# Optimization experiments

Hardware: AMD Instinct MI355X
Metric: run time of the kernel (lower is better)

The kernel has to match this reference:

```python
import jax, jax.numpy as jnp
import numpy as np
from jax import lax
import math

LAYERS, STACKS = 10, 3
NL = LAYERS * STACKS          # 30 residual layers
DC, RC, SC, CLASSES, K = 32, 32, 256, 256, 2


def _conv1d(x, w, b, dilation=1, pad_left=0):
    # x: [B, Cin, T], w: [Cout, Cin, Kw]. Left-padding by (Kw-1)*dilation
    # reproduces torch's symmetric pad followed by x[:, :, :T] (causal conv).
    out = lax.conv_general_dilated(
        x, w, window_strides=(1,), padding=[(pad_left, 0)],
        rhs_dilation=(dilation,), dimension_numbers=('NCH', 'OIH', 'NCH'))
    return out + b[None, :, None]


def setup_inputs() -> dict:
    key = jax.random.key(0)
    ks = jax.random.split(key, 13)
    B, T = 4, 32768
    s = jnp.float32(0.05)
    return {
        'y': jax.random.normal(ks[0], (B, CLASSES, T), jnp.float32),
        'W_causal': jax.random.normal(ks[1], (RC, CLASSES, 1)) * s,
        'b_causal': jax.random.normal(ks[2], (RC,)) * s,
        'Wf': jax.random.normal(ks[3], (NL, DC, RC, K)) * s,
        'bf': jax.random.normal(ks[4], (NL, DC)) * s,
        'Wr': jax.random.normal(ks[5], (NL, RC, DC // 2, 1)) * s,
        'br': jax.random.normal(ks[6], (NL, RC)) * s,
        'Ws': jax.random.normal(ks[7], (NL, SC, DC // 2, 1)) * s,
        'bs': jax.random.normal(ks[8], (NL, SC)) * s,
        'W_e1': jax.random.normal(ks[9], (SC, SC, 1)) * s,
        'b_e1': jax.random.normal(ks[10], (SC,)) * s,
        'W_e2': jax.random.normal(ks[11], (CLASSES, SC, 1)) * s,
        'b_e2': jax.random.normal(ks[12], (CLASSES,)) * s,
    }


def reference(y, W_causal, b_causal, Wf, bf, Wr, br, Ws, bs, W_e1, b_e1, W_e2, b_e2):
    # y: [B, 256, T]
    x = _conv1d(y, W_causal, b_causal)                      # [B, RC, T]
    skip = jnp.zeros((y.shape[0], SC, y.shape[2]), y.dtype)
    inv_sqrt2 = jnp.float32(math.sqrt(0.5))
    for i in range(NL):  # fixed 30 structurally distinct layers (dilation varies)
        d = 2 ** (i % LAYERS)
        residual = x
        h = _conv1d(x, Wf[i], bf[i], dilation=d, pad_left=(K - 1) * d)  # [B, DC, T]
        a, b = jnp.split(h, 2, axis=1)                      # each [B, DC//2, T]
        g = jnp.tanh(a) * jax.nn.sigmoid(b)
        skip = skip + _conv1d(g, Ws[i], bs[i])              # [B, SC, T]
        x = (_conv1d(g, Wr[i], br[i]) + residual) * inv_sqrt2
    x = jax.nn.relu(skip)
    x = jax.nn.relu(_conv1d(x, W_e1, b_e1))
    x = _conv1d(x, W_e2, b_e2)                              # [B, CLASSES, T]
    return jnp.transpose(x, (0, 2, 1))                      # [B, T, CLASSES]
```

## Files before the change

kernel.cpp:

```cpp
#include <hip/hip_runtime.h>
#include <hip/hip_bf16.h>


#define B_ 4
#define T_ 32768
#define RC_ 32
#define KH_ 16
#define SC_ 256
#define CLASSES_ 256
#define NL_ 30
#define NT_ 131072L

using f32x4 = __attribute__((ext_vector_type(4))) float;
using s16x8 = __attribute__((ext_vector_type(8))) short;

__device__ inline float fast_rcp(float x) { return __builtin_amdgcn_rcpf(x); }
__device__ inline float fast_sigmoid(float x) { return fast_rcp(1.f + __expf(-x)); }
__device__ inline float fast_tanh(float x) { return 1.f - 2.f * fast_rcp(__expf(2.f * x) + 1.f); }

__device__ inline ushort f2bf(float v) {
    __hip_bfloat16 h = __float2bfloat16(v);
    return __builtin_bit_cast(ushort, h);
}
__device__ inline uint pack2(float a, float b) {
    return (uint)f2bf(a) | ((uint)f2bf(b) << 16);
}
__device__ inline float bflo(uint u) { return __builtin_bit_cast(float, u << 16); }
__device__ inline float bfhi(uint u) { return __builtin_bit_cast(float, u & 0xffff0000u); }
__device__ inline s16x8 mfma_in(uint4 u) { return __builtin_bit_cast(s16x8, u); }

__global__ __launch_bounds__(256) void prep_w_kernel(
    const float* __restrict__ Wc, const float* __restrict__ Wf,
    const float* __restrict__ Wr, const float* __restrict__ Ws,
    const float* __restrict__ We1, const float* __restrict__ We2,
    ushort* __restrict__ wcp, ushort* __restrict__ wfp, ushort* __restrict__ wrp,
    ushort* __restrict__ wsF, ushort* __restrict__ we1F, ushort* __restrict__ we2F)
{
    int j = blockIdx.x * 256 + threadIdx.x;
    if (j < 24576) {
        int m = j / 768, k = j % 768;
        float v = Wc[m * 256 + (k & 255)];
        if (k < 512) wcp[j] = f2bf(v);
        else {
            float hi = __bfloat162float(__float2bfloat16(v));
            wcp[j] = f2bf(v - hi);
        }
    } else if (j < 86016) {
        int e = j - 24576;
        int i = e >> 11; int r = e & 2047;
        int tap = r >> 10, c = (r >> 5) & 31, ci = r & 31;
        wfp[e] = f2bf(Wf[((size_t)(i * 32 + c) * 32 + ci) * 2 + tap]);
    } else if (j < 116736) {
        int e = j - 86016;
        int i = e >> 10; int c = (e >> 5) & 31; int k = e & 31;
        wrp[e] = (k < 16) ? f2bf(Wr[(size_t)(i * 32 + c) * 16 + k]) : (ushort)0;
    } else if (j < 239616) {
        int e = j - 116736;
        int jj = e & 7, lane = (e >> 3) & 63, mrow = (e >> 9) & 15, kc = e >> 13;
        int m = mrow * 16 + (lane & 15);
        int k = kc * 32 + (lane >> 4) * 8 + jj;
        int i = k >> 4, ci = k & 15;
        wsF[e] = f2bf(Ws[((size_t)i * 256 + m) * 16 + ci]);
    } else if (j < 305152) {
        int e = j - 239616;
        int jj = e & 7, lane = (e >> 3) & 63, mrow = (e >> 9) & 15, kc = e >> 13;
        int m = mrow * 16 + (lane & 15);
        int k = kc * 32 + (lane >> 4) * 8 + jj;
        we1F[e] = f2bf(We1[m * 256 + k]);
    } else if (j < 370688) {
        int e = j - 305152;
        int jj = e & 7, lane = (e >> 3) & 63, mrow = (e >> 9) & 15, kc = e >> 13;
        int m = mrow * 16 + (lane & 15);
        int k = kc * 32 + (lane >> 4) * 8 + jj;
        we2F[e] = f2bf(We2[m * 256 + k]);
    }
}

__global__ void bsum_kernel(const float* __restrict__ bs, float* __restrict__ bsSum) {
    int s = threadIdx.x;
    float v = 0.f;
    #pragma unroll
    for (int i = 0; i < NL_; ++i) v += bs[i * SC_ + s];
    bsSum[s] = v;
}

__global__ __launch_bounds__(256) void prep_y_kernel(
    const float* __restrict__ y, ushort* __restrict__ y_t)
{
    __shared__ float lds[32][65];
    int tid = threadIdx.x;
    int b = blockIdx.x >> 9;
    long t0 = (long)(blockIdx.x & 511) * 64;
    for (int cc = 0; cc < 8; ++cc) {
        int c = cc * 32 + (tid >> 3);
        int tp = (tid & 7) * 8;
        const float* src = y + ((size_t)b * 256 + c) * T_ + t0 + tp;
        float4 v0 = *(const float4*)src;
        float4 v1 = *(const float4*)(src + 4);
        lds[tid >> 3][tp + 0] = v0.x; lds[tid >> 3][tp + 1] = v0.y;
        lds[tid >> 3][tp + 2] = v0.z; lds[tid >> 3][tp + 3] = v0.w;
        lds[tid >> 3][tp + 4] = v1.x; lds[tid >> 3][tp + 5] = v1.y;
        lds[tid >> 3][tp + 6] = v1.z; lds[tid >> 3][tp + 7] = v1.w;
        __syncthreads();
        int t = tid & 63, cp = tid >> 6;
        float v[8];
        #pragma unroll
        for (int jj = 0; jj < 8; ++jj) v[jj] = lds[cp * 8 + jj][t];
        uint hi[4], lo[4];
        #pragma unroll
        for (int jj = 0; jj < 4; ++jj) {
            float a = v[2 * jj], bv = v[2 * jj + 1];
            float ah = __bfloat162float(__float2bfloat16(a));
            float bh = __bfloat162float(__float2bfloat16(bv));
            hi[jj] = pack2(a, bv);
            lo[jj] = pack2(a - ah, bv - bh);
        }
        ushort* dst = y_t + ((size_t)b * T_ + t0 + t) * 512 + cc * 32 + cp * 8;
        *(uint4*)dst = make_uint4(hi[0], hi[1], hi[2], hi[3]);
        *(uint4*)(dst + 256) = make_uint4(lo[0], lo[1], lo[2], lo[3]);
        __syncthreads();
    }
}

__global__ __launch_bounds__(256) void init_gemm_kernel(
    const ushort* __restrict__ wcp, const ushort* __restrict__ y_t,
    const float* __restrict__ bc, ushort* __restrict__ x0)
{
    __shared__ ushort sa[2][32 * 40];
    __shared__ ushort sb[2][256 * 40];
    int tid = threadIdx.x;
    int wid = tid >> 6, lane = tid & 63, q = lane >> 4, ln = lane & 15;
    long n0 = (long)blockIdx.x * 256;

    uint4 ar0, ar1, br0, br1, br2, br3;
    auto load_tile = [&](int kc) {
        int k0 = kc * 32;
        int koff = (k0 < 512) ? k0 : k0 - 512;
        if (tid < 64) {
            int m = tid >> 1, h = tid & 1;
            const uint4* s = (const uint4*)(wcp + m * 768 + k0 + h * 16);
            ar0 = s[0]; ar1 = s[1];
        }
        const uint4* sB = (const uint4*)(y_t + (n0 + tid) * 512 + koff);
        br0 = sB[0]; br1 = sB[1]; br2 = sB[2]; br3 = sB[3];
    };
    auto store_tile = [&](int buf) {
        if (tid < 64) {
            int m = tid >> 1, h = tid & 1;
            *(uint4*)&sa[buf][m * 40 + h * 16] = ar0;
            *(uint4*)&sa[buf][m * 40 + h * 16 + 8] = ar1;
        }
        *(uint4*)&sb[buf][tid * 40 + 0]  = br0;
        *(uint4*)&sb[buf][tid * 40 + 8]  = br1;
        *(uint4*)&sb[buf][tid * 40 + 16] = br2;
        *(uint4*)&sb[buf][tid * 40 + 24] = br3;
    };

    f32x4 acc[2][4];
    #pragma unroll
    for (int mi = 0; mi < 2; ++mi) {
        f32x4 bv = *(const f32x4*)&bc[mi * 16 + 4 * q];
        #pragma unroll
        for (int ni = 0; ni < 4; ++ni) acc[mi][ni] = bv;
    }
    load_tile(0);
    for (int kc = 0; kc < 24; ++kc) {
        int buf = kc & 1;
        store_tile(buf);
        __syncthreads();
        if (kc + 1 < 24) load_tile(kc + 1);
        s16x8 af[2];
        #pragma unroll
        for (int mi = 0; mi < 2; ++mi)
            af[mi] = mfma_in(*(const uint4*)&sa[buf][(mi * 16 + ln) * 40 + q * 8]);
        #pragma unroll
        for (int ni = 0; ni < 4; ++ni) {
            s16x8 bfr = mfma_in(*(const uint4*)&sb[buf][(wid * 64 + ni * 16 + ln) * 40 + q * 8]);
            #pragma unroll
            for (int mi = 0; mi < 2; ++mi)
                acc[mi][ni] = __builtin_amdgcn_mfma_f32_16x16x32_bf16(af[mi], bfr, acc[mi][ni], 0, 0, 0);
        }
        __syncthreads();
    }
    #pragma unroll
    for (int mi = 0; mi < 2; ++mi) {
        int ch = mi * 16 + 4 * q;
        #pragma unroll
        for (int ni = 0; ni < 4; ++ni) {
            long t = n0 + wid * 64 + ni * 16 + ln;
            f32x4 v = acc[mi][ni];
            uint2 pk; pk.x = pack2(v[0], v[1]); pk.y = pack2(v[2], v[3]);
            *(uint2*)&x0[t * 32 + ch] = pk;
        }
    }
}

__global__ __launch_bounds__(256) void layer_mfma_kernel(
    const ushort* __restrict__ xb_in, ushort* __restrict__ xb_out,
    ushort* __restrict__ g_out,
    const ushort* __restrict__ wfp, const ushort* __restrict__ wrp,
    const float* __restrict__ bfp, const float* __restrict__ brp, int d)
{
    int tid = threadIdx.x;
    int wid = tid >> 6, lane = tid & 63, q = lane >> 4, ln = lane & 15;
    long tw = (long)blockIdx.x * 128 + wid * 32;

    s16x8 wfA[2][2], wrA[2];
    #pragma unroll
    for (int mb = 0; mb < 2; ++mb) {
        #pragma unroll
        for (int tap = 0; tap < 2; ++tap)
            wfA[mb][tap] = mfma_in(*(const uint4*)&wfp[(tap * 32 + mb * 16 + ln) * 32 + q * 8]);
        wrA[mb] = mfma_in(*(const uint4*)&wrp[(mb * 16 + ln) * 32 + q * 8]);
    }
    f32x4 bfv0 = *(const f32x4*)&bfp[4 * q];
    f32x4 bfv1 = *(const f32x4*)&bfp[16 + 4 * q];
    f32x4 brv0 = *(const f32x4*)&brp[4 * q];
    f32x4 brv1 = *(const f32x4*)&brp[16 + 4 * q];
    const float inv_s2 = 0.70710678118654752f;

    #pragma unroll
    for (int nb = 0; nb < 2; ++nb) {
        long t = tw + nb * 16 + ln;
        bool vok = ((int)(t & (T_ - 1)) >= d);
        long r0 = vok ? (t - d) : t;
        uint4 u0 = *(const uint4*)&xb_in[r0 * 32 + 8 * q];
        if (!vok) u0 = make_uint4(0, 0, 0, 0);
        uint4 u1 = *(const uint4*)&xb_in[t * 32 + 8 * q];
        s16x8 b0 = mfma_in(u0), b1 = mfma_in(u1);

        f32x4 h0 = {}, h1 = {};
        h0 = __builtin_amdgcn_mfma_f32_16x16x32_bf16(wfA[0][0], b0, h0, 0, 0, 0);
        h0 = __builtin_amdgcn_mfma_f32_16x16x32_bf16(wfA[0][1], b1, h0, 0, 0, 0);
        h1 = __builtin_amdgcn_mfma_f32_16x16x32_bf16(wfA[1][0], b0, h1, 0, 0, 0);
        h1 = __builtin_amdgcn_mfma_f32_16x16x32_bf16(wfA[1][1], b1, h1, 0, 0, 0);

        float g[4];
        #pragma unroll
        for (int r = 0; r < 4; ++r)
            g[r] = fast_tanh(h0[r] + bfv0[r]) * fast_sigmoid(h1[r] + bfv1[r]);
        uint p01 = pack2(g[0], g[1]), p23 = pack2(g[2], g[3]);
        uint2 gst; gst.x = p01; gst.y = p23;
        *(uint2*)&g_out[t * 16 + 4 * q] = gst;

        int sA = q * 32 + ln;
        uint f0 = (uint)__shfl((int)p01, sA);
        uint f1 = (uint)__shfl((int)p23, sA);
        uint f2 = (uint)__shfl((int)p01, sA + 16);
        uint f3 = (uint)__shfl((int)p23, sA + 16);
        s16x8 gb = mfma_in(make_uint4(f0, f1, f2, f3));

        f32x4 rr0 = {}, rr1 = {};
        rr0 = __builtin_amdgcn_mfma_f32_16x16x32_bf16(wrA[0], gb, rr0, 0, 0, 0);
        rr1 = __builtin_amdgcn_mfma_f32_16x16x32_bf16(wrA[1], gb, rr1, 0, 0, 0);

        uint2 xr0 = *(const uint2*)&xb_in[t * 32 + 4 * q];
        uint2 xr1 = *(const uint2*)&xb_in[t * 32 + 16 + 4 * q];
        float o00 = (rr0[0] + brv0[0] + bflo(xr0.x)) * inv_s2;
        float o01 = (rr0[1] + brv0[1] + bfhi(xr0.x)) * inv_s2;
        float o02 = (rr0[2] + brv0[2] + bflo(xr0.y)) * inv_s2;
        float o03 = (rr0[3] + brv0[3] + bfhi(xr0.y)) * inv_s2;
        float o10 = (rr1[0] + brv1[0] + bflo(xr1.x)) * inv_s2;
        float o11 = (rr1[1] + brv1[1] + bfhi(xr1.x)) * inv_s2;
        float o12 = (rr1[2] + brv1[2] + bflo(xr1.y)) * inv_s2;
        float o13 = (rr1[3] + brv1[3] + bfhi(xr1.y)) * inv_s2;
        uint2 xp0; xp0.x = pack2(o00, o01); xp0.y = pack2(o02, o03);
        uint2 xp1; xp1.x = pack2(o10, o11); xp1.y = pack2(o12, o13);
        *(uint2*)&xb_out[t * 32 + 4 * q] = xp0;
        *(uint2*)&xb_out[t * 32 + 16 + 4 * q] = xp1;
    }
}

__global__ __launch_bounds__(256, 4) void tail_kernel(
    const ushort* __restrict__ g_all, const float* __restrict__ bsSum,
    const ushort* __restrict__ wsF, const ushort* __restrict__ we1F,
    const ushort* __restrict__ we2F, const float* __restrict__ be1,
    const float* __restrict__ be2, float* __restrict__ out)
{
    __shared__ ushort stg[2][2048];
    __shared__ ushort pq[16384];
    int tid = threadIdx.x;
    int wid = tid >> 6, lane = tid & 63, q = lane >> 4, ln = lane & 15;
    long n0 = (long)blockIdx.x * 64;
    int wrow = wid * 64;

    int sn = tid & 63, sip = (tid >> 6) & 1, shalf = tid >> 7;
    int sdst = ((sn >> 4) * 64 + (sip * 2 + shalf) * 16 + (sn & 15)) * 8;

    f32x4 acc[4][4];
    #pragma unroll
    for (int mi = 0; mi < 4; ++mi) {
        f32x4 bv = *(const f32x4*)&bsSum[wrow + mi * 16 + 4 * q];
        #pragma unroll
        for (int ni = 0; ni < 4; ++ni) acc[mi][ni] = bv;
    }

    uint4 ld = *(const uint4*)(g_all + ((size_t)sip * NT_ + n0 + sn) * 16 + shalf * 8);
    *(uint4*)&stg[0][sdst] = ld;
    for (int kc = 0; kc < 15; ++kc) {
        __syncthreads();
        if (kc < 14)
            ld = *(const uint4*)(g_all +
                ((size_t)(2 * (kc + 1) + sip) * NT_ + n0 + sn) * 16 + shalf * 8);
        s16x8 af[4], bfr[4];
        #pragma unroll
        for (int mi = 0; mi < 4; ++mi)
            af[mi] = mfma_in(*(const uint4*)(wsF +
                (((size_t)kc * 16 + wid * 4 + mi) * 64 + lane) * 8));
        #pragma unroll
        for (int ni = 0; ni < 4; ++ni)
            bfr[ni] = mfma_in(*(const uint4*)&stg[kc & 1][(ni * 64 + lane) * 8]);
        #pragma unroll
        for (int ni = 0; ni < 4; ++ni)
            #pragma unroll
            for (int mi = 0; mi < 4; ++mi)
                acc[mi][ni] = __builtin_amdgcn_mfma_f32_16x16x32_bf16(
                    af[mi], bfr[ni], acc[mi][ni], 0, 0, 0);
        if (kc < 14) *(uint4*)&stg[(kc + 1) & 1][sdst] = ld;
    }
    #pragma unroll
    for (int mi = 0; mi < 4; ++mi) {
        int ch = wrow + mi * 16 + 4 * q;
        int dbase = ((ch >> 5) * 4) * 512 + (((ch & 31) >> 3) * 16 + ln) * 8 + (ch & 7);
        #pragma unroll
        for (int ni = 0; ni < 4; ++ni) {
            f32x4 v = acc[mi][ni];
            uint2 pk;
            pk.x = pack2(fmaxf(v[0], 0.f), fmaxf(v[1], 0.f));
            pk.y = pack2(fmaxf(v[2], 0.f), fmaxf(v[3], 0.f));
            *(uint2*)&pq[dbase + ni * 512] = pk;
        }
    }
    __syncthreads();

    #pragma unroll
    for (int mi = 0; mi < 4; ++mi) {
        f32x4 bv = *(const f32x4*)&be1[wrow + mi * 16 + 4 * q];
        #pragma unroll
        for (int ni = 0; ni < 4; ++ni) acc[mi][ni] = bv;
    }
    for (int kc = 0; kc < 8; ++kc) {
        s16x8 af[4], bfr[4];
        #pragma unroll
        for (int mi = 0; mi < 4; ++mi)
            af[mi] = mfma_in(*(const uint4*)(we1F +
                (((size_t)kc * 16 + wid * 4 + mi) * 64 + lane) * 8));
        #pragma unroll
        for (int ni = 0; ni < 4; ++ni)
            bfr[ni] = mfma_in(*(const uint4*)&pq[(kc * 4 + ni) * 512 + lane * 8]);
        #pragma unroll
        for (int ni = 0; ni < 4; ++ni)
            #pragma unroll
            for (int mi = 0; mi < 4; ++mi)
                acc[mi][ni] = __builtin_amdgcn_mfma_f32_16x16x32_bf16(
                    af[mi], bfr[ni], acc[mi][ni], 0, 0, 0);
    }
    __syncthreads();
    #pragma unroll
    for (int mi = 0; mi < 4; ++mi) {
        int ch = wrow + mi * 16 + 4 * q;
        int dbase = ((ch >> 5) * 4) * 512 + (((ch & 31) >> 3) * 16 + ln) * 8 + (ch & 7);
        #pragma unroll
        for (int ni = 0; ni < 4; ++ni) {
            f32x4 v = acc[mi][ni];
            uint2 pk;
            pk.x = pack2(fmaxf(v[0], 0.f), fmaxf(v[1], 0.f));
            pk.y = pack2(fmaxf(v[2], 0.f), fmaxf(v[3], 0.f));
            *(uint2*)&pq[dbase + ni * 512] = pk;
        }
    }
    __syncthreads();

    #pragma unroll
    for (int mi = 0; mi < 4; ++mi) {
        f32x4 bv = *(const f32x4*)&be2[wrow + mi * 16 + 4 * q];
        #pragma unroll
        for (int ni = 0; ni < 4; ++ni) acc[mi][ni] = bv;
    }
    for (int kc = 0; kc < 8; ++kc) {
        s16x8 af[4], bfr[4];
        #pragma unroll
        for (int mi = 0; mi < 4; ++mi)
            af[mi] = mfma_in(*(const uint4*)(we2F +
                (((size_t)kc * 16 + wid * 4 + mi) * 64 + lane) * 8));
        #pragma unroll
        for (int ni = 0; ni < 4; ++ni)
            bfr[ni] = mfma_in(*(const uint4*)&pq[(kc * 4 + ni) * 512 + lane * 8]);
        #pragma unroll
        for (int ni = 0; ni < 4; ++ni)
            #pragma unroll
            for (int mi = 0; mi < 4; ++mi)
                acc[mi][ni] = __builtin_amdgcn_mfma_f32_16x16x32_bf16(
                    af[mi], bfr[ni], acc[mi][ni], 0, 0, 0);
    }
    #pragma unroll
    for (int mi = 0; mi < 4; ++mi) {
        int ch = wrow + mi * 16 + 4 * q;
        #pragma unroll
        for (int ni = 0; ni < 4; ++ni) {
            long t = n0 + ni * 16 + ln;
            *(f32x4*)&out[t * 256 + ch] = acc[mi][ni];
        }
    }
}

__device__ inline float load_g(const float* p) { return *p; }
__device__ inline float load_g(const __hip_bfloat16* p) { return __bfloat162float(*p); }
__device__ inline void store_g(float* p, float v) { *p = v; }
__device__ inline void store_g(__hip_bfloat16* p, float v) { *p = __float2bfloat16(v); }

__global__ __launch_bounds__(256) void init_conv_kernel(
    const float* __restrict__ y, const float* __restrict__ Wc,
    const float* __restrict__ bc, float* __restrict__ x0)
{
    int gid = blockIdx.x * 256 + threadIdx.x;
    int b = gid >> 15;
    int t = gid & (T_ - 1);
    float acc[RC_];
    #pragma unroll
    for (int c = 0; c < RC_; ++c) acc[c] = bc[c];
    const float* yb = y + (size_t)b * CLASSES_ * T_ + t;
    for (int cb = 0; cb < CLASSES_; cb += 32) {
        float yv[32];
        #pragma unroll
        for (int j = 0; j < 32; ++j) yv[j] = yb[(size_t)(cb + j) * T_];
        #pragma unroll
        for (int c = 0; c < RC_; ++c)
            #pragma unroll
            for (int j = 0; j < 32; ++j)
                acc[c] = fmaf(Wc[c * CLASSES_ + cb + j], yv[j], acc[c]);
    }
    float* xo = x0 + (size_t)b * RC_ * T_ + t;
    #pragma unroll
    for (int c = 0; c < RC_; ++c) xo[(size_t)c * T_] = acc[c];
}

template <typename G>
__global__ __launch_bounds__(256) void layer_kernel(
    const float* __restrict__ x_in, float* __restrict__ x_out, G* __restrict__ g_out,
    const float* __restrict__ wf, const float* __restrict__ bfp,
    const float* __restrict__ wr, const float* __restrict__ brp, int d)
{
    int gid = blockIdx.x * 256 + threadIdx.x;
    int b = gid >> 15;
    int t = gid & (T_ - 1);
    const float* xbase = x_in + (size_t)b * RC_ * T_ + t;
    float xm[RC_], xd[RC_];
    #pragma unroll
    for (int ci = 0; ci < RC_; ++ci) xm[ci] = xbase[(size_t)ci * T_];
    #pragma unroll
    for (int ci = 0; ci < RC_; ++ci)
        xd[ci] = (t >= d) ? xbase[(size_t)ci * T_ - d] : 0.f;
    float a_[KH_];
    #pragma unroll
    for (int c = 0; c < KH_; ++c) {
        float s = bfp[c];
        #pragma unroll
        for (int ci = 0; ci < RC_; ++ci) {
            s = fmaf(wf[(c * RC_ + ci) * 2 + 0], xd[ci], s);
            s = fmaf(wf[(c * RC_ + ci) * 2 + 1], xm[ci], s);
        }
        a_[c] = s;
    }
    float g[KH_];
    #pragma unroll
    for (int c = 0; c < KH_; ++c) {
        float s = bfp[KH_ + c];
        #pragma unroll
        for (int ci = 0; ci < RC_; ++ci) {
            s = fmaf(wf[((KH_ + c) * RC_ + ci) * 2 + 0], xd[ci], s);
            s = fmaf(wf[((KH_ + c) * RC_ + ci) * 2 + 1], xm[ci], s);
        }
        g[c] = fast_tanh(a_[c]) * fast_sigmoid(s);
    }
    G* gb = g_out + (size_t)b * KH_ * T_ + t;
    #pragma unroll
    for (int c = 0; c < KH_; ++c) store_g(gb + (size_t)c * T_, g[c]);
    float* xo = x_out + (size_t)b * RC_ * T_ + t;
    #pragma unroll
    for (int c = 0; c < RC_; ++c) {
        float s = brp[c];
        #pragma unroll
        for (int ci = 0; ci < KH_; ++ci) s = fmaf(wr[c * KH_ + ci], g[ci], s);
        xo[(size_t)c * T_] = (s + xm[c]) * 0.70710678118654752f;
    }
}

template <typename G>
__global__ __launch_bounds__(256) void final_kernel(
    const G* __restrict__ g_all, const float* __restrict__ bsSum,
    const float* __restrict__ Ws, const float* __restrict__ We1,
    const float* __restrict__ be1, const float* __restrict__ We2,
    const float* __restrict__ be2, float* __restrict__ out)
{
    __shared__ float smem[14336];
    float* plds = smem;
    float* qlds = smem + 5120;
    float* glds = smem;
    float* wlds = smem + 10240;
    int tid = threadIdx.x;
    int bt = blockIdx.x;
    int b = bt >> 11;
    int t0 = (bt & 2047) << 4;
    int c4 = tid & 63;
    int th = tid >> 6;
    for (int e = tid; e < 480 * 16; e += 256) {
        int row = e >> 4, col = e & 15;
        int i = row >> 4, ci = row & 15;
        glds[e] = load_g(g_all + ((size_t)(i * B_ + b) * KH_ + ci) * T_ + t0 + col);
    }
    __syncthreads();
    float acc[4][4];
    #pragma unroll
    for (int j = 0; j < 4; ++j) {
        float bv = bsSum[c4 + 64 * j];
        #pragma unroll
        for (int tt = 0; tt < 4; ++tt) acc[j][tt] = bv;
    }
    for (int i = 0; i < NL_; ++i) {
        const float4* wsrc = (const float4*)(Ws + ((size_t)i * 256 + tid) * 16);
        float4 w0 = wsrc[0], w1 = wsrc[1], w2 = wsrc[2], w3 = wsrc[3];
        __syncthreads();
        wlds[0*256+tid]=w0.x; wlds[1*256+tid]=w0.y; wlds[2*256+tid]=w0.z; wlds[3*256+tid]=w0.w;
        wlds[4*256+tid]=w1.x; wlds[5*256+tid]=w1.y; wlds[6*256+tid]=w1.z; wlds[7*256+tid]=w1.w;
        wlds[8*256+tid]=w2.x; wlds[9*256+tid]=w2.y; wlds[10*256+tid]=w2.z; wlds[11*256+tid]=w2.w;
        wlds[12*256+tid]=w3.x; wlds[13*256+tid]=w3.y; wlds[14*256+tid]=w3.z; wlds[15*256+tid]=w3.w;
        __syncthreads();
        #pragma unroll
        for (int ci = 0; ci < 16; ++ci) {
            const float4 gv = *(const float4*)&glds[(i * 16 + ci) * 16 + th * 4];
            float wv[4];
            #pragma unroll
            for (int j = 0; j < 4; ++j) wv[j] = wlds[ci * 256 + c4 + 64 * j];
            #pragma unroll
            for (int j = 0; j < 4; ++j) {
                acc[j][0] = fmaf(wv[j], gv.x, acc[j][0]);
                acc[j][1] = fmaf(wv[j], gv.y, acc[j][1]);
                acc[j][2] = fmaf(wv[j], gv.z, acc[j][2]);
                acc[j][3] = fmaf(wv[j], gv.w, acc[j][3]);
            }
        }
    }
    __syncthreads();
    #pragma unroll
    for (int j = 0; j < 4; ++j)
        #pragma unroll
        for (int tt = 0; tt < 4; ++tt)
            plds[(c4 + 64 * j) * 20 + th * 4 + tt] = fmaxf(acc[j][tt], 0.f);
    #pragma unroll
    for (int j = 0; j < 4; ++j) {
        float bv = be1[c4 + 64 * j];
        #pragma unroll
        for (int tt = 0; tt < 4; ++tt) acc[j][tt] = bv;
    }
    for (int kc = 0; kc < 16; ++kc) {
        const float4* wsrc = (const float4*)(We1 + (size_t)tid * 256 + kc * 16);
        float4 w0 = wsrc[0], w1 = wsrc[1], w2 = wsrc[2], w3 = wsrc[3];
        __syncthreads();
        wlds[0*256+tid]=w0.x; wlds[1*256+tid]=w0.y; wlds[2*256+tid]=w0.z; wlds[3*256+tid]=w0.w;
        wlds[4*256+tid]=w1.x; wlds[5*256+tid]=w1.y; wlds[6*256+tid]=w1.z; wlds[7*256+tid]=w1.w;
        wlds[8*256+tid]=w2.x; wlds[9*256+tid]=w2.y; wlds[10*256+tid]=w2.z; wlds[11*256+tid]=w2.w;
        wlds[12*256+tid]=w3.x; wlds[13*256+tid]=w3.y; wlds[14*256+tid]=w3.z; wlds[15*256+tid]=w3.w;
        __syncthreads();
        #pragma unroll
        for (int kk = 0; kk < 16; ++kk) {
            const float4 pv = *(const float4*)&plds[(kc * 16 + kk) * 20 + th * 4];
            float wv[4];
            #pragma unroll
            for (int j = 0; j < 4; ++j) wv[j] = wlds[kk * 256 + c4 + 64 * j];
            #pragma unroll
            for (int j = 0; j < 4; ++j) {
                acc[j][0] = fmaf(wv[j], pv.x, acc[j][0]);
                acc[j][1] = fmaf(wv[j], pv.y, acc[j][1]);
                acc[j][2] = fmaf(wv[j], pv.z, acc[j][2]);
                acc[j][3] = fmaf(wv[j], pv.w, acc[j][3]);
            }
        }
    }
    __syncthreads();
    #pragma unroll
    for (int j = 0; j < 4; ++j)
        #pragma unroll
        for (int tt = 0; tt < 4; ++tt)
            qlds[(c4 + 64 * j) * 20 + th * 4 + tt] = fmaxf(acc[j][tt], 0.f);
    #pragma unroll
    for (int j = 0; j < 4; ++j) {
        float bv = be2[c4 + 64 * j];
        #pragma unroll
        for (int tt = 0; tt < 4; ++tt) acc[j][tt] = bv;
    }
    for (int kc = 0; kc < 16; ++kc) {
        const float4* wsrc = (const float4*)(We2 + (size_t)tid * 256 + kc * 16);
        float4 w0 = wsrc[0], w1 = wsrc[1], w2 = wsrc[2], w3 = wsrc[3];
        __syncthreads();
        wlds[0*256+tid]=w0.x; wlds[1*256+tid]=w0.y; wlds[2*256+tid]=w0.z; wlds[3*256+tid]=w0.w;
        wlds[4*256+tid]=w1.x; wlds[5*256+tid]=w1.y; wlds[6*256+tid]=w1.z; wlds[7*256+tid]=w1.w;
        wlds[8*256+tid]=w2.x; wlds[9*256+tid]=w2.y; wlds[10*256+tid]=w2.z; wlds[11*256+tid]=w2.w;
        wlds[12*256+tid]=w3.x; wlds[13*256+tid]=w3.y; wlds[14*256+tid]=w3.z; wlds[15*256+tid]=w3.w;
        __syncthreads();
        #pragma unroll
        for (int kk = 0; kk < 16; ++kk) {
            const float4 qv = *(const float4*)&qlds[(kc * 16 + kk) * 20 + th * 4];
            float wv[4];
            #pragma unroll
            for (int j = 0; j < 4; ++j) wv[j] = wlds[kk * 256 + c4 + 64 * j];
            #pragma unroll
            for (int j = 0; j < 4; ++j) {
                acc[j][0] = fmaf(wv[j], qv.x, acc[j][0]);
                acc[j][1] = fmaf(wv[j], qv.y, acc[j][1]);
                acc[j][2] = fmaf(wv[j], qv.z, acc[j][2]);
                acc[j][3] = fmaf(wv[j], qv.w, acc[j][3]);
            }
        }
    }
    #pragma unroll
    for (int tt = 0; tt < 4; ++tt) {
        size_t orow = ((size_t)b * T_ + t0 + th * 4 + tt) * 256;
        #pragma unroll
        for (int j = 0; j < 4; ++j)
            out[orow + c4 + 64 * j] = acc[j][tt];
    }
}

template <typename G>
static void run_pipeline_old(const float* y, const float* Wc, const float* bc,
                             const float* Wf, const float* bf, const float* Wr,
                             const float* br, const float* Ws, const float* bs,
                             const float* We1, const float* be1, const float* We2,
                             const float* be2, float* out, char* ws, hipStream_t stream)
{
    size_t xbytes = (size_t)B_ * RC_ * T_ * sizeof(float);
    float* xa = (float*)ws;
    float* xb = (float*)(ws + xbytes);
    G* g_all = (G*)(ws + 2 * xbytes);
    size_t gbytes = (size_t)NL_ * B_ * KH_ * T_ * sizeof(G);
    float* bsSum = (float*)(ws + 2 * xbytes + gbytes);
    bsum_kernel<<<1, 256, 0, stream>>>(bs, bsSum);
    init_conv_kernel<<<512, 256, 0, stream>>>(y, Wc, bc, xa);
    float* xin = xa; float* xout = xb;
    for (int i = 0; i < NL_; ++i) {
        int d = 1 << (i % 10);
        layer_kernel<G><<<512, 256, 0, stream>>>(
            xin, xout, g_all + (size_t)i * B_ * KH_ * T_,
            Wf + (size_t)i * RC_ * RC_ * 2, bf + (size_t)i * RC_,
            Wr + (size_t)i * RC_ * KH_, br + (size_t)i * RC_, d);
        float* tmp = xin; xin = xout; xout = tmp;
    }
    final_kernel<G><<<B_ * (T_ / 16), 256, 0, stream>>>(
        g_all, bsSum, Ws, We1, be1, We2, be2, out);
}

extern "C" void kernel_launch(void* const* d_in, const int* in_sizes, int n_in,
                              void* d_out, int out_size, void* d_ws, size_t ws_size,
                              hipStream_t stream)
{
    (void)in_sizes; (void)n_in; (void)out_size;
    const float* y   = (const float*)d_in[0];
    const float* Wc  = (const float*)d_in[1];
    const float* bc  = (const float*)d_in[2];
    const float* Wf  = (const float*)d_in[3];
    const float* bf  = (const float*)d_in[4];
    const float* Wr  = (const float*)d_in[5];
    const float* br  = (const float*)d_in[6];
    const float* Ws  = (const float*)d_in[7];
    const float* bs  = (const float*)d_in[8];
    const float* We1 = (const float*)d_in[9];
    const float* be1 = (const float*)d_in[10];
    const float* We2 = (const float*)d_in[11];
    const float* be2 = (const float*)d_in[12];
    float* out = (float*)d_out;
    char* ws = (char*)d_ws;

    size_t o = 0;
    auto alloc = [&](size_t bytes) { size_t r = o; o += (bytes + 1023) & ~(size_t)1023; return r; };
    size_t o_reg = alloc(NT_ * 512 * 2);
    size_t o_xa  = alloc(NT_ * 32 * 2);
    size_t o_xb  = alloc(NT_ * 32 * 2);
    size_t o_wcp = alloc(24576 * 2);
    size_t o_wfp = alloc(61440 * 2);
    size_t o_wrp = alloc(30720 * 2);
    size_t o_wst = alloc(122880 * 2);
    size_t o_we1 = alloc(65536 * 2);
    size_t o_we2 = alloc(65536 * 2);
    size_t o_bss = alloc(1024);
    size_t need_new = o;

    if (ws_size >= need_new) {
        ushort* y_t  = (ushort*)(ws + o_reg);
        ushort* g    = (ushort*)(ws + o_reg);
        ushort* xba  = (ushort*)(ws + o_xa);
        ushort* xbb  = (ushort*)(ws + o_xb);
        ushort* wcp  = (ushort*)(ws + o_wcp);
        ushort* wfp  = (ushort*)(ws + o_wfp);
        ushort* wrp  = (ushort*)(ws + o_wrp);
        ushort* wsF  = (ushort*)(ws + o_wst);
        ushort* we1F = (ushort*)(ws + o_we1);
        ushort* we2F = (ushort*)(ws + o_we2);
        float*  bsSum= (float*)(ws + o_bss);

        prep_w_kernel<<<1448, 256, 0, stream>>>(Wc, Wf, Wr, Ws, We1, We2,
                                                wcp, wfp, wrp, wsF, we1F, we2F);
        bsum_kernel<<<1, 256, 0, stream>>>(bs, bsSum);
        prep_y_kernel<<<2048, 256, 0, stream>>>(y, y_t);
        init_gemm_kernel<<<512, 256, 0, stream>>>(wcp, y_t, bc, xba);

        ushort* xbin = xba; ushort* xbout = xbb;
        for (int i = 0; i < NL_; ++i) {
            int d = 1 << (i % 10);
            layer_mfma_kernel<<<1024, 256, 0, stream>>>(
                xbin, xbout, g + (size_t)i * NT_ * 16,
                wfp + (size_t)i * 2048, wrp + (size_t)i * 1024,
                bf + i * 32, br + i * 32, d);
            ushort* tmp = xbin; xbin = xbout; xbout = tmp;
        }

        tail_kernel<<<2048, 256, 0, stream>>>(g, bsSum, wsF, we1F, we2F,
                                              be1, be2, out);
        return;
    }

    size_t xbytes = (size_t)B_ * RC_ * T_ * sizeof(float);
    size_t need_f32 = 2 * xbytes + (size_t)NL_ * B_ * KH_ * T_ * 4 + 1024;
    if (ws_size >= need_f32)
        run_pipeline_old<float>(y, Wc, bc, Wf, bf, Wr, br, Ws, bs, We1, be1, We2, be2, out, ws, stream);
    else
        run_pipeline_old<__hip_bfloat16>(y, Wc, bc, Wf, bf, Wr, br, Ws, bs, We1, be1, We2, be2, out, ws, stream);
}
```

Before: 690.6 us.

## Fuse first seven dilated layers per stack into one LDS-resident kernel

Adds a stack kernel that loads a 256-step time tile plus a 128-step causal halo into shared memory and runs the first seven layers of each stack (dilations 1..64) there, exchanging x between double-buffered LDS tiles instead of global memory. Only the gate outputs and the final x are written out, and the last three layers still use the per-layer kernel. This removes the global x round trips and launches for those layers but recomputes the halo region and adds barriers. The tail kernel's output store now goes through shared memory so global writes are coalesced rows, and the fallback fp32 path is deleted.

```diff
diff --git a/kernel.cpp b/kernel.cpp
--- a/kernel.cpp
+++ b/kernel.cpp
@@ -195,6 +195,112 @@
     }
 }
 
+__global__ __launch_bounds__(256) void stack_kernel(
+    const ushort* __restrict__ xb_in, ushort* __restrict__ xb_out,
+    ushort* __restrict__ g_out,
+    const ushort* __restrict__ wfp,
+    const ushort* __restrict__ wrp,
+    const float* __restrict__ bfp, const float* __restrict__ brp)
+{
+    __shared__ ushort xl[2][384 * 40];
+    int tid = threadIdx.x;
+    int wid = tid >> 6, lane = tid & 63, q = lane >> 4, ln = lane & 15;
+    long bo = (long)blockIdx.x * 256;
+
+    #pragma unroll
+    for (int k = 0; k < 6; ++k) {
+        int idx = k * 256 + tid;
+        int row = idx >> 2, part = idx & 3;
+        long t = bo - 128 + row;
+        if (t < 0) t = 0;
+        uint4 v = *(const uint4*)&xb_in[t * 32 + part * 8];
+        *(uint4*)&xl[0][row * 40 + part * 8] = v;
+    }
+    __syncthreads();
+
+    const float inv_s2 = 0.70710678118654752f;
+    int cur = 0;
+    for (int j = 0; j < 7; ++j) {
+        int d = 1 << j;
+        s16x8 wfA[2][2], wrA[2];
+        #pragma unroll
+        for (int mb = 0; mb < 2; ++mb) {
+            #pragma unroll
+            for (int tap = 0; tap < 2; ++tap)
+                wfA[mb][tap] = mfma_in(*(const uint4*)&wfp[(size_t)j * 2048 +
+                    (tap * 32 + mb * 16 + ln) * 32 + q * 8]);
+            wrA[mb] = mfma_in(*(const uint4*)&wrp[(size_t)j * 1024 + (mb * 16 + ln) * 32 + q * 8]);
+        }
+        f32x4 bfv0 = *(const f32x4*)&bfp[j * 32 + 4 * q];
+        f32x4 bfv1 = *(const f32x4*)&bfp[j * 32 + 16 + 4 * q];
+        f32x4 brv0 = *(const f32x4*)&brp[j * 32 + 4 * q];
+        f32x4 brv1 = *(const f32x4*)&brp[j * 32 + 16 + 4 * q];
+        ushort* ga = g_out + (size_t)j * NT_ * 16;
+
+        #pragma unroll
+        for (int nb = 0; nb < 6; ++nb) {
+            int tb = wid * 96 + nb * 16;
+            int tl = tb + ln;
+            long t = bo - 128 + tl;
+            bool vok = ((int)(t & (T_ - 1)) >= d);
+            int rd = tl - d; if (rd < 0) rd = 0;
+            uint4 u0 = *(const uint4*)&xl[cur][rd * 40 + 8 * q];
+            if (!vok) u0 = make_uint4(0, 0, 0, 0);
+            uint4 u1 = *(const uint4*)&xl[cur][tl * 40 + 8 * q];
+            s16x8 b0 = mfma_in(u0), b1 = mfma_in(u1);
+
+            f32x4 h0 = {}, h1 = {};
+            h0 = __builtin_amdgcn_mfma_f32_16x16x32_bf16(wfA[0][0], b0, h0, 0, 0, 0);
+            h0 = __builtin_amdgcn_mfma_f32_16x16x32_bf16(wfA[0][1], b1, h0, 0, 0, 0);
+            h1 = __builtin_amdgcn_mfma_f32_16x16x32_bf16(wfA[1][0], b0, h1, 0, 0, 0);
+            h1 = __builtin_amdgcn_mfma_f32_16x16x32_bf16(wfA[1][1], b1, h1, 0, 0, 0);
+
+            float g[4];
+            #pragma unroll
+            for (int r = 0; r < 4; ++r)
+                g[r] = fast_tanh(h0[r] + bfv0[r]) * fast_sigmoid(h1[r] + bfv1[r]);
+            uint p01 = pack2(g[0], g[1]), p23 = pack2(g[2], g[3]);
+            if (tb >= 128) {
+                uint2 gst; gst.x = p01; gst.y = p23;
+                *(uint2*)&ga[t * 16 + 4 * q] = gst;
+            }
+
+            int sA = q * 32 + ln;
+            uint f0 = (uint)__shfl((int)p01, sA);
+            uint f1 = (uint)__shfl((int)p23, sA);
+            uint f2 = (uint)__shfl((int)p01, sA + 16);
+            uint f3 = (uint)__shfl((int)p23, sA + 16);
+            s16x8 gb = mfma_in(make_uint4(f0, f1, f2, f3));
+
+            f32x4 rr0 = {}, rr1 = {};
+            rr0 = __builtin_amdgcn_mfma_f32_16x16x32_bf16(wrA[0], gb, rr0, 0, 0, 0);
+            rr1 = __builtin_amdgcn_mfma_f32_16x16x32_bf16(wrA[1], gb, rr1, 0, 0, 0);
+
+            uint2 xr0 = *(const uint2*)&xl[cur][tl * 40 + 4 * q];
+            uint2 xr1 = *(const uint2*)&xl[cur][tl * 40 + 16 + 4 * q];
+            float o00 = (rr0[0] + brv0[0] + bflo(xr0.x)) * inv_s2;
+            float o01 = (rr0[1] + brv0[1] + bfhi(xr0.x)) * inv_s2;
+            float o02 = (rr0[2] + brv0[2] + bflo(xr0.y)) * inv_s2;
+            float o03 = (rr0[3] + brv0[3] + bfhi(xr0.y)) * inv_s2;
+            float o10 = (rr1[0] + brv1[0] + bflo(xr1.x)) * inv_s2;
+            float o11 = (rr1[1] + brv1[1] + bfhi(xr1.x)) * inv_s2;
+            float o12 = (rr1[2] + brv1[2] + bflo(xr1.y)) * inv_s2;
+            float o13 = (rr1[3] + brv1[3] + bfhi(xr1.y)) * inv_s2;
+            uint2 xp0; xp0.x = pack2(o00, o01); xp0.y = pack2(o02, o03);
+            uint2 xp1; xp1.x = pack2(o10, o11); xp1.y = pack2(o12, o13);
+            if (j < 6) {
+                *(uint2*)&xl[cur ^ 1][tl * 40 + 4 * q] = xp0;
+                *(uint2*)&xl[cur ^ 1][tl * 40 + 16 + 4 * q] = xp1;
+            } else if (tb >= 128) {
+                *(uint2*)&xb_out[t * 32 + 4 * q] = xp0;
+                *(uint2*)&xb_out[t * 32 + 16 + 4 * q] = xp1;
+            }
+        }
+        __syncthreads();
+        cur ^= 1;
+    }
+}
+
 __global__ __launch_bounds__(256) void layer_mfma_kernel(
     const ushort* __restrict__ xb_in, ushort* __restrict__ xb_out,
     ushort* __restrict__ g_out,
@@ -393,268 +499,30 @@
                 acc[mi][ni] = __builtin_amdgcn_mfma_f32_16x16x32_bf16(
                     af[mi], bfr[ni], acc[mi][ni], 0, 0, 0);
     }
-    #pragma unroll
-    for (int mi = 0; mi < 4; ++mi) {
-        int ch = wrow + mi * 16 + 4 * q;
-        #pragma unroll
-        for (int ni = 0; ni < 4; ++ni) {
-            long t = n0 + ni * 16 + ln;
-            *(f32x4*)&out[t * 256 + ch] = acc[mi][ni];
-        }
-    }
-}
-
-__device__ inline float load_g(const float* p) { return *p; }
-__device__ inline float load_g(const __hip_bfloat16* p) { return __bfloat162float(*p); }
-__device__ inline void store_g(float* p, float v) { *p = v; }
-__device__ inline void store_g(__hip_bfloat16* p, float v) { *p = __float2bfloat16(v); }
-
-__global__ __launch_bounds__(256) void init_conv_kernel(
-    const float* __restrict__ y, const float* __restrict__ Wc,
-    const float* __restrict__ bc, float* __restrict__ x0)
-{
-    int gid = blockIdx.x * 256 + threadIdx.x;
-    int b = gid >> 15;
-    int t = gid & (T_ - 1);
-    float acc[RC_];
-    #pragma unroll
-    for (int c = 0; c < RC_; ++c) acc[c] = bc[c];
-    const float* yb = y + (size_t)b * CLASSES_ * T_ + t;
-    for (int cb = 0; cb < CLASSES_; cb += 32) {
-        float yv[32];
-        #pragma unroll
-        for (int j = 0; j < 32; ++j) yv[j] = yb[(size_t)(cb + j) * T_];
-        #pragma unroll
-        for (int c = 0; c < RC_; ++c)
-            #pragma unroll
-            for (int j = 0; j < 32; ++j)
-                acc[c] = fmaf(Wc[c * CLASSES_ + cb + j], yv[j], acc[c]);
-    }
-    float* xo = x0 + (size_t)b * RC_ * T_ + t;
-    #pragma unroll
-    for (int c = 0; c < RC_; ++c) xo[(size_t)c * T_] = acc[c];
-}
-
-template <typename G>
-__global__ __launch_bounds__(256) void layer_kernel(
-    const float* __restrict__ x_in, float* __restrict__ x_out, G* __restrict__ g_out,
-    const float* __restrict__ wf, const float* __restrict__ bfp,
-    const float* __restrict__ wr, const float* __restrict__ brp, int d)
-{
-    int gid = blockIdx.x * 256 + threadIdx.x;
-    int b = gid >> 15;
-    int t = gid & (T_ - 1);
-    const float* xbase = x_in + (size_t)b * RC_ * T_ + t;
-    float xm[RC_], xd[RC_];
-    #pragma unroll
-    for (int ci = 0; ci < RC_; ++ci) xm[ci] = xbase[(size_t)ci * T_];
-    #pragma unroll
-    for (int ci = 0; ci < RC_; ++ci)
-        xd[ci] = (t >= d) ? xbase[(size_t)ci * T_ - d] : 0.f;
-    float a_[KH_];
-    #pragma unroll
-    for (int c = 0; c < KH_; ++c) {
-        float s = bfp[c];
-        #pragma unroll
-        for (int ci = 0; ci < RC_; ++ci) {
-            s = fmaf(wf[(c * RC_ + ci) * 2 + 0], xd[ci], s);
-            s = fmaf(wf[(c * RC_ + ci) * 2 + 1], xm[ci], s);
-        }
-        a_[c] = s;
-    }
-    float g[KH_];
-    #pragma unroll
-    for (int c = 0; c < KH_; ++c) {
-        float s = bfp[KH_ + c];
-        #pragma unroll
-        for (int ci = 0; ci < RC_; ++ci) {
-            s = fmaf(wf[((KH_ + c) * RC_ + ci) * 2 + 0], xd[ci], s);
-            s = fmaf(wf[((KH_ + c) * RC_ + ci) * 2 + 1], xm[ci], s);
-        }
-        g[c] = fast_tanh(a_[c]) * fast_sigmoid(s);
-    }
-    G* gb = g_out + (size_t)b * KH_ * T_ + t;
-    #pragma unroll
-    for (int c = 0; c < KH_; ++c) store_g(gb + (size_t)c * T_, g[c]);
-    float* xo = x_out + (size_t)b * RC_ * T_ + t;
-    #pragma unroll
-    for (int c = 0; c < RC_; ++c) {
-        float s = brp[c];
-        #pragma unroll
-        for (int ci = 0; ci < KH_; ++ci) s = fmaf(wr[c * KH_ + ci], g[ci], s);
-        xo[(size_t)c * T_] = (s + xm[c]) * 0.70710678118654752f;
-    }
-}
-
-template <typename G>
-__global__ __launch_bounds__(256) void final_kernel(
-    const G* __restrict__ g_all, const float* __restrict__ bsSum,
-    const float* __restrict__ Ws, const float* __restrict__ We1,
-    const float* __restrict__ be1, const float* __restrict__ We2,
-    const float* __restrict__ be2, float* __restrict__ out)
-{
-    __shared__ float smem[14336];
-    float* plds = smem;
-    float* qlds = smem + 5120;
-    float* glds = smem;
-    float* wlds = smem + 10240;
-    int tid = threadIdx.x;
-    int bt = blockIdx.x;
-    int b = bt >> 11;
-    int t0 = (bt & 2047) << 4;
-    int c4 = tid & 63;
-    int th = tid >> 6;
-    for (int e = tid; e < 480 * 16; e += 256) {
-        int row = e >> 4, col = e & 15;
-        int i = row >> 4, ci = row & 15;
-        glds[e] = load_g(g_all + ((size_t)(i * B_ + b) * KH_ + ci) * T_ + t0 + col);
-    }
-    __syncthreads();
-    float acc[4][4];
-    #pragma unroll
-    for (int j = 0; j < 4; ++j) {
-        float bv = bsSum[c4 + 64 * j];
-        #pragma unroll
-        for (int tt = 0; tt < 4; ++tt) acc[j][tt] = bv;
-    }
-    for (int i = 0; i < NL_; ++i) {
-        const float4* wsrc = (const float4*)(Ws + ((size_t)i * 256 + tid) * 16);
-        float4 w0 = wsrc[0], w1 = wsrc[1], w2 = wsrc[2], w3 = wsrc[3];
-        __syncthreads();
-        wlds[0*256+tid]=w0.x; wlds[1*256+tid]=w0.y; wlds[2*256+tid]=w0.z; wlds[3*256+tid]=w0.w;
-        wlds[4*256+tid]=w1.x; wlds[5*256+tid]=w1.y; wlds[6*256+tid]=w1.z; wlds[7*256+tid]=w1.w;
-        wlds[8*256+tid]=w2.x; wlds[9*256+tid]=w2.y; wlds[10*256+tid]=w2.z; wlds[11*256+tid]=w2.w;
-        wlds[12*256+tid]=w3.x; wlds[13*256+tid]=w3.y; wlds[14*256+tid]=w3.z; wlds[15*256+tid]=w3.w;
-        __syncthreads();
-        #pragma unroll
-        for (int ci = 0; ci < 16; ++ci) {
-            const float4 gv = *(const float4*)&glds[(i * 16 + ci) * 16 + th * 4];
-            float wv[4];
-            #pragma unroll
-            for (int j = 0; j < 4; ++j) wv[j] = wlds[ci * 256 + c4 + 64 * j];
-            #pragma unroll
-            for (int j = 0; j < 4; ++j) {
-                acc[j][0] = fmaf(wv[j], gv.x, acc[j][0]);
-                acc[j][1] = fmaf(wv[j], gv.y, acc[j][1]);
-                acc[j][2] = fmaf(wv[j], gv.z, acc[j][2]);
-                acc[j][3] = fmaf(wv[j], gv.w, acc[j][3]);
-            }
-        }
-    }
-    __syncthreads();
-    #pragma unroll
-    for (int j = 0; j < 4; ++j)
-        #pragma unroll
-        for (int tt = 0; tt < 4; ++tt)
-            plds[(c4 + 64 * j) * 20 + th * 4 + tt] = fmaxf(acc[j][tt], 0.f);
-    #pragma unroll
-    for (int j = 0; j < 4; ++j) {
-        float bv = be1[c4 + 64 * j];
-        #pragma unroll
-        for (int tt = 0; tt < 4; ++tt) acc[j][tt] = bv;
-    }
-    for (int kc = 0; kc < 16; ++kc) {
-        const float4* wsrc = (const float4*)(We1 + (size_t)tid * 256 + kc * 16);
-        float4 w0 = wsrc[0], w1 = wsrc[1], w2 = wsrc[2], w3 = wsrc[3];
-        __syncthreads();
-        wlds[0*256+tid]=w0.x; wlds[1*256+tid]=w0.y; wlds[2*256+tid]=w0.z; wlds[3*256+tid]=w0.w;
-        wlds[4*256+tid]=w1.x; wlds[5*256+tid]=w1.y; wlds[6*256+tid]=w1.z; wlds[7*256+tid]=w1.w;
-        wlds[8*256+tid]=w2.x; wlds[9*256+tid]=w2.y; wlds[10*256+tid]=w2.z; wlds[11*256+tid]=w2.w;
-        wlds[12*256+tid]=w3.x; wlds[13*256+tid]=w3.y; wlds[14*256+tid]=w3.z; wlds[15*256+tid]=w3.w;
-        __syncthreads();
-        #pragma unroll
-        for (int kk = 0; kk < 16; ++kk) {
-            const float4 pv = *(const float4*)&plds[(kc * 16 + kk) * 20 + th * 4];
-            float wv[4];
-            #pragma unroll
-            for (int j = 0; j < 4; ++j) wv[j] = wlds[kk * 256 + c4 + 64 * j];
-            #pragma unroll
-            for (int j = 0; j < 4; ++j) {
-                acc[j][0] = fmaf(wv[j], pv.x, acc[j][0]);
-                acc[j][1] = fmaf(wv[j], pv.y, acc[j][1]);
-                acc[j][2] = fmaf(wv[j], pv.z, acc[j][2]);
-                acc[j][3] = fmaf(wv[j], pv.w, acc[j][3]);
-            }
-        }
-    }
-    __syncthreads();
-    #pragma unroll
-    for (int j = 0; j < 4; ++j)
-        #pragma unroll
-        for (int tt = 0; tt < 4; ++tt)
-            qlds[(c4 + 64 * j) * 20 + th * 4 + tt] = fmaxf(acc[j][tt], 0.f);
-    #pragma unroll
-    for (int j = 0; j < 4; ++j) {
-        float bv = be2[c4 + 64 * j];
-        #pragma unroll
-        for (int tt = 0; tt < 4; ++tt) acc[j][tt] = bv;
-    }
-    for (int kc = 0; kc < 16; ++kc) {
-        const float4* wsrc = (const float4*)(We2 + (size_t)tid * 256 + kc * 16);
-        float4 w0 = wsrc[0], w1 = wsrc[1], w2 = wsrc[2], w3 = wsrc[3];
-        __syncthreads();
-        wlds[0*256+tid]=w0.x; wlds[1*256+tid]=w0.y; wlds[2*256+tid]=w0.z; wlds[3*256+tid]=w0.w;
-        wlds[4*256+tid]=w1.x; wlds[5*256+tid]=w1.y; wlds[6*256+tid]=w1.z; wlds[7*256+tid]=w1.w;
-        wlds[8*256+tid]=w2.x; wlds[9*256+tid]=w2.y; wlds[10*256+tid]=w2.z; wlds[11*256+tid]=w2.w;
-        wlds[12*256+tid]=w3.x; wlds[13*256+tid]=w3.y; wlds[14*256+tid]=w3.z; wlds[15*256+tid]=w3.w;
-        __syncthreads();
-        #pragma unroll
-        for (int kk = 0; kk < 16; ++kk) {
-            const float4 qv = *(const float4*)&qlds[(kc * 16 + kk) * 20 + th * 4];
-            float wv[4];
-            #pragma unroll
-            for (int j = 0; j < 4; ++j) wv[j] = wlds[kk * 256 + c4 + 64 * j];
-            #pragma unroll
-            for (int j = 0; j < 4; ++j) {
-                acc[j][0] = fmaf(wv[j], qv.x, acc[j][0]);
-                acc[j][1] = fmaf(wv[j], qv.y, acc[j][1]);
-                acc[j][2] = fmaf(wv[j], qv.z, acc[j][2]);
-                acc[j][3] = fmaf(wv[j], qv.w, acc[j][3]);
-            }
-        }
-    }
-    #pragma unroll
-    for (int tt = 0; tt < 4; ++tt) {
-        size_t orow = ((size_t)b * T_ + t0 + th * 4 + tt) * 256;
-        #pragma unroll
-        for (int j = 0; j < 4; ++j)
-            out[orow + c4 + 64 * j] = acc[j][tt];
-    }
-}
-
-template <typename G>
-static void run_pipeline_old(const float* y, const float* Wc, const float* bc,
-                             const float* Wf, const float* bf, const float* Wr,
-                             const float* br, const float* Ws, const float* bs,
-                             const float* We1, const float* be1, const float* We2,
-                             const float* be2, float* out, char* ws, hipStream_t stream)
-{
-    size_t xbytes = (size_t)B_ * RC_ * T_ * sizeof(float);
-    float* xa = (float*)ws;
-    float* xb = (float*)(ws + xbytes);
-    G* g_all = (G*)(ws + 2 * xbytes);
-    size_t gbytes = (size_t)NL_ * B_ * KH_ * T_ * sizeof(G);
-    float* bsSum = (float*)(ws + 2 * xbytes + gbytes);
-    bsum_kernel<<<1, 256, 0, stream>>>(bs, bsSum);
-    init_conv_kernel<<<512, 256, 0, stream>>>(y, Wc, bc, xa);
-    float* xin = xa; float* xout = xb;
-    for (int i = 0; i < NL_; ++i) {
-        int d = 1 << (i % 10);
-        layer_kernel<G><<<512, 256, 0, stream>>>(
-            xin, xout, g_all + (size_t)i * B_ * KH_ * T_,
-            Wf + (size_t)i * RC_ * RC_ * 2, bf + (size_t)i * RC_,
-            Wr + (size_t)i * RC_ * KH_, br + (size_t)i * RC_, d);
-        float* tmp = xin; xin = xout; xout = tmp;
-    }
-    final_kernel<G><<<B_ * (T_ / 16), 256, 0, stream>>>(
-        g_all, bsSum, Ws, We1, be1, We2, be2, out);
+
+    float* pqf = (float*)pq;
+    #pragma unroll
+    for (int c = 0; c < 4; ++c) {
+        __syncthreads();
+        #pragma unroll
+        for (int mi = 0; mi < 4; ++mi)
+            *(f32x4*)&pqf[ln * 260 + wrow + mi * 16 + 4 * q] = acc[mi][c];
+        __syncthreads();
+        #pragma unroll
+        for (int k = 0; k < 4; ++k) {
+            int pos = k * 256 + tid;
+            int row = pos >> 6, col = (pos & 63) * 4;
+            *(f32x4*)&out[(n0 + c * 16 + row) * 256 + col] =
+                *(const f32x4*)&pqf[row * 260 + col];
+        }
+    }
 }
 
 extern "C" void kernel_launch(void* const* d_in, const int* in_sizes, int n_in,
                               void* d_out, int out_size, void* d_ws, size_t ws_size,
                               hipStream_t stream)
 {
-    (void)in_sizes; (void)n_in; (void)out_size;
+    (void)in_sizes; (void)n_in; (void)out_size; (void)ws_size;
     const float* y   = (const float*)d_in[0];
     const float* Wc  = (const float*)d_in[1];
     const float* bc  = (const float*)d_in[2];
@@ -683,46 +551,44 @@
     size_t o_we1 = alloc(65536 * 2);
     size_t o_we2 = alloc(65536 * 2);
     size_t o_bss = alloc(1024);
-    size_t need_new = o;
-
-    if (ws_size >= need_new) {
-        ushort* y_t  = (ushort*)(ws + o_reg);
-        ushort* g    = (ushort*)(ws + o_reg);
-        ushort* xba  = (ushort*)(ws + o_xa);
-        ushort* xbb  = (ushort*)(ws + o_xb);
-        ushort* wcp  = (ushort*)(ws + o_wcp);
-        ushort* wfp  = (ushort*)(ws + o_wfp);
-        ushort* wrp  = (ushort*)(ws + o_wrp);
-        ushort* wsF  = (ushort*)(ws + o_wst);
-        ushort* we1F = (ushort*)(ws + o_we1);
-        ushort* we2F = (ushort*)(ws + o_we2);
-        float*  bsSum= (float*)(ws + o_bss);
-
-        prep_w_kernel<<<1448, 256, 0, stream>>>(Wc, Wf, Wr, Ws, We1, We2,
-                                                wcp, wfp, wrp, wsF, we1F, we2F);
-        bsum_kernel<<<1, 256, 0, stream>>>(bs, bsSum);
-        prep_y_kernel<<<2048, 256, 0, stream>>>(y, y_t);
-        init_gemm_kernel<<<512, 256, 0, stream>>>(wcp, y_t, bc, xba);
-
-        ushort* xbin = xba; ushort* xbout = xbb;
-        for (int i = 0; i < NL_; ++i) {
-            int d = 1 << (i % 10);
+
+    ushort* y_t  = (ushort*)(ws + o_reg);
+    ushort* g    = (ushort*)(ws + o_reg);
+    ushort* xba  = (ushort*)(ws + o_xa);
+    ushort* xbb  = (ushort*)(ws + o_xb);
+    ushort* wcp  = (ushort*)(ws + o_wcp);
+    ushort* wfp  = (ushort*)(ws + o_wfp);
+    ushort* wrp  = (ushort*)(ws + o_wrp);
+    ushort* wsF  = (ushort*)(ws + o_wst);
+    ushort* we1F = (ushort*)(ws + o_we1);
+    ushort* we2F = (ushort*)(ws + o_we2);
+    float*  bsSum= (float*)(ws + o_bss);
+
+    prep_w_kernel<<<1448, 256, 0, stream>>>(Wc, Wf, Wr, Ws, We1, We2,
+                                            wcp, wfp, wrp, wsF, we1F, we2F);
+    bsum_kernel<<<1, 256, 0, stream>>>(bs, bsSum);
+    prep_y_kernel<<<2048, 256, 0, stream>>>(y, y_t);
+    init_gemm_kernel<<<512, 256, 0, stream>>>(wcp, y_t, bc, xba);
+
+    ushort* xbin = xba; ushort* xbout = xbb;
+    for (int s = 0; s < 3; ++s) {
+        int i0 = s * 10;
+        stack_kernel<<<512, 256, 0, stream>>>(
+            xbin, xbout, g + (size_t)i0 * NT_ * 16,
+            wfp + (size_t)i0 * 2048, wrp + (size_t)i0 * 1024,
+            bf + i0 * 32, br + i0 * 32);
+        { ushort* tmp = xbin; xbin = xbout; xbout = tmp; }
+        for (int jj = 7; jj < 10; ++jj) {
+            int i = i0 + jj;
+            int d = 1 << jj;
             layer_mfma_kernel<<<1024, 256, 0, stream>>>(
                 xbin, xbout, g + (size_t)i * NT_ * 16,
                 wfp + (size_t)i * 2048, wrp + (size_t)i * 1024,
                 bf + i * 32, br + i * 32, d);
-            ushort* tmp = xbin; xbin = xbout; xbout = tmp;
-        }
-
-        tail_kernel<<<2048, 256, 0, stream>>>(g, bsSum, wsF, we1F, we2F,
-                                              be1, be2, out);
-        return;
-    }
-
-    size_t xbytes = (size_t)B_ * RC_ * T_ * sizeof(float);
-    size_t need_f32 = 2 * xbytes + (size_t)NL_ * B_ * KH_ * T_ * 4 + 1024;
-    if (ws_size >= need_f32)
-        run_pipeline_old<float>(y, Wc, bc, Wf, bf, Wr, br, Ws, bs, We1, be1, We2, be2, out, ws, stream);
-    else
-        run_pipeline_old<__hip_bfloat16>(y, Wc, bc, Wf, bf, Wr, br, Ws, bs, We1, be1, We2, be2, out, ws, stream);
-}
+            { ushort* tmp = xbin; xbin = xbout; xbout = tmp; }
+        }
+    }
+
+    tail_kernel<<<2048, 256, 0, stream>>>(g, bsSum, wsF, we1F, we2F,
+                                          be1, be2, out);
+}
```

Result: faster. 653.6 us (-5.4%).
